# Optimization experiments

Measured on AMD Instinct MI355X. Metric: run time of the kernel, lower is better.

The kernel has to match this reference:

```python
import jax, jax.numpy as jnp
import numpy as np

TEMP = 1.0  # softmax temperature (init kwarg)


def setup_inputs() -> dict:
    key = jax.random.key(0)
    k1, k2 = jax.random.split(key)
    two_n, d_model = 512, 256
    embeddings = jax.random.normal(k1, (two_n, d_model), dtype=jnp.float32)
    targets = jax.random.uniform(k2, (two_n, 1), dtype=jnp.float32)
    return {"embeddings": embeddings, "targets": targets}


def reference(embeddings, targets):
    # embeddings: [2N, d_model], targets: [2N, 1]
    two_n = embeddings.shape[0]
    # label distance d[i,j] = |t_i - t_j|
    d = jnp.abs(targets - targets.T)                                  # [2N, 2N]
    # exp similarity s[i,j] = exp(-||e_i - e_j||_2 / temp)
    diff = embeddings[:, None, :] - embeddings[None, :, :]            # [2N, 2N, d]
    s = jnp.exp(-jnp.linalg.norm(diff, axis=-1) / TEMP)               # [2N, 2N]
    off_diag = 1.0 - jnp.eye(two_n, dtype=s.dtype)                    # [2N, 2N]
    # mask3[i,k,j] = (d[i,j] >= d[i,k]) * (j != i)
    mask3 = (d[:, None, :] >= d[:, :, None]).astype(s.dtype) * off_diag[:, None, :]
    # denominator D[i,k] = sum_j mask3[i,k,j] * s[i,j]
    denom = jnp.einsum('ikj,ij->ik', mask3, s)                        # [2N, 2N]
    loss = jnp.log(s / denom) * off_diag
    return -jnp.sum(loss) / (two_n * (two_n - 1))
```

## Files before the change

kernel.cpp:

```cpp
#include <hip/hip_runtime.h>
#include <math.h>

#define TWO_N 512
#define DM    256
#define NT    256
#define NTR   512
#define KS    8
#define RSTRIDE (TWO_N * TWO_N)

#define OFF_TSORT (8u << 20)
#define OFF_INV   ((8u << 20) + 2048)
#define OFF_BSUM  ((8u << 20) + 4096)

#define ACC4(acc, A, B) { float _d;                      \
    _d = (A).x - (B).x; acc += _d * _d;                  \
    _d = (A).y - (B).y; acc += _d * _d;                  \
    _d = (A).z - (B).z; acc += _d * _d;                  \
    _d = (A).w - (B).w; acc += _d * _d; }

__global__ __launch_bounds__(NT) void supcr_dist_rank(
    const float* __restrict__ E, const float* __restrict__ T,
    float* __restrict__ R, float* __restrict__ tsort, int* __restrict__ inv)
{
    const int bid = blockIdx.x;
    const int t   = threadIdx.x;

    if (bid < 512) {
        __shared__ float4 As4[64 * 9];
        __shared__ float4 Bs4[64 * 9];
        const int tile = bid >> 3, ks = bid & 7;
        const int it = tile >> 3, jt = tile & 7;
        const float4* __restrict__ E4 = reinterpret_cast<const float4*>(E);

        #pragma unroll
        for (int p = 0; p < 2; ++p) {
            const int idx = t + p * 256;
            const int r = idx >> 3, c4 = idx & 7;
            As4[r * 9 + c4] = E4[(it * 64 + r) * 64 + ks * 8 + c4];
            Bs4[r * 9 + c4] = E4[(jt * 64 + r) * 64 + ks * 8 + c4];
        }
        __syncthreads();

        const int tx = t & 15, ty = t >> 4;
        float acc[4][4];
        #pragma unroll
        for (int u = 0; u < 4; ++u)
            #pragma unroll
            for (int v = 0; v < 4; ++v) acc[u][v] = 0.f;

        #pragma unroll
        for (int k4 = 0; k4 < 8; ++k4) {
            float4 a[4], b[4];
            #pragma unroll
            for (int u = 0; u < 4; ++u) a[u] = As4[(ty + 16 * u) * 9 + k4];
            #pragma unroll
            for (int v = 0; v < 4; ++v) b[v] = Bs4[(tx + 16 * v) * 9 + k4];
            #pragma unroll
            for (int u = 0; u < 4; ++u)
                #pragma unroll
                for (int v = 0; v < 4; ++v) ACC4(acc[u][v], a[u], b[v]);
        }

        float* __restrict__ Rp = R + (size_t)ks * RSTRIDE;
        #pragma unroll
        for (int u = 0; u < 4; ++u) {
            const int row = it * 64 + ty + 16 * u;
            #pragma unroll
            for (int v = 0; v < 4; ++v)
                Rp[row * TWO_N + jt * 64 + tx + 16 * v] = acc[u][v];
        }
    } else {
        __shared__ float Tsh[TWO_N];
        Tsh[t] = T[t]; Tsh[t + 256] = T[t + 256];
        __syncthreads();

        const int ja = t, jb = t + 256;
        const float ta = Tsh[ja], tb = Tsh[jb];
        int rka = 0, rkb = 0;
        const float4* Tsh4 = reinterpret_cast<const float4*>(Tsh);
        #pragma unroll 4
        for (int j4 = 0; j4 < TWO_N / 4; ++j4) {
            const float4 tv = Tsh4[j4];
            const int b0 = 4 * j4, b1 = b0 + 1, b2 = b0 + 2, b3 = b0 + 3;
            rka += (tv.x < ta) || (tv.x == ta && b0 < ja);
            rka += (tv.y < ta) || (tv.y == ta && b1 < ja);
            rka += (tv.z < ta) || (tv.z == ta && b2 < ja);
            rka += (tv.w < ta) || (tv.w == ta && b3 < ja);
            rkb += (tv.x < tb) || (tv.x == tb && b0 < jb);
            rkb += (tv.y < tb) || (tv.y == tb && b1 < jb);
            rkb += (tv.z < tb) || (tv.z == tb && b2 < jb);
            rkb += (tv.w < tb) || (tv.w == tb && b3 < jb);
        }
        tsort[rka] = ta;  inv[ja] = rka;
        tsort[rkb] = tb;  inv[jb] = rkb;
    }
}

__global__ __launch_bounds__(NTR) void supcr_rows(
    const float* __restrict__ T, const float* __restrict__ R,
    const float* __restrict__ tsort, const int* __restrict__ inv,
    double* __restrict__ bsums)
{
    const int i = blockIdx.x;
    const int k = threadIdx.x;
    const int lane = k & 63, wid = k >> 6;

    __shared__ float  ts[TWO_N];
    __shared__ float  Pe[TWO_N];
    __shared__ float  P[TWO_N];
    __shared__ float  wsumf[8];
    __shared__ double red8[8];

    const float ti = T[i];
    const float tk = T[k];

    float d2 = 0.f;
    #pragma unroll
    for (int p = 0; p < KS; ++p)
        d2 += R[(size_t)p * RSTRIDE + (size_t)i * TWO_N + k];
    const float rik = sqrtf(d2);
    const float e   = (k == i) ? 0.f : __expf(-rik);

    ts[k] = tsort[k];
    Pe[inv[k]] = e;
    __syncthreads();

    float v = Pe[k];
    #pragma unroll
    for (int off = 1; off < 64; off <<= 1) {
        const float u = __shfl_up(v, off, 64);
        if (lane >= off) v += u;
    }
    if (lane == 63) wsumf[wid] = v;
    __syncthreads();
    float base = 0.f, tot = 0.f;
    #pragma unroll
    for (int w = 0; w < 8; ++w) {
        const float s = wsumf[w];
        tot += s;
        if (w < wid) base += s;
    }
    P[k] = v + base;
    const float Stot = tot;
    __syncthreads();

    const int mi = inv[i];

    double local = 0.0;
    if (k != i) {
        const float theta = fabsf(ti - tk);

        const int nl = mi + 1;
        int pos = 0;
        #pragma unroll
        for (int step = 512; step >= 1; step >>= 1) {
            const int np = pos + step;
            if (np <= nl && fabsf(ti - ts[np - 1]) >= theta) pos = np;
        }
        const int cl = nl - pos;

        const int nr = TWO_N - mi;
        int pr = 0;
        #pragma unroll
        for (int step = 512; step >= 1; step >>= 1) {
            const int np = pr + step;
            if (np <= nr && fabsf(ti - ts[mi + np - 1]) < theta) pr = np;
        }
        const int cr = pr;

        float inner = 0.f;
        const int L  = mi - cl + 1;
        const int Rr = mi + cr - 1;
        if (Rr >= L) inner = P[Rr] - ((L > 0) ? P[L - 1] : 0.f);
        const float denom = Stot - inner;
        local = (double)(-rik - logf(denom));
    }

    #pragma unroll
    for (int off = 32; off > 0; off >>= 1) local += __shfl_down(local, off, 64);
    if (lane == 0) red8[wid] = local;
    __syncthreads();
    if (k == 0) {
        double s = 0.0;
        #pragma unroll
        for (int w = 0; w < 8; ++w) s += red8[w];
        bsums[i] = s;
    }
}

__global__ __launch_bounds__(64) void supcr_finalize(
    const double* __restrict__ bsums, float* __restrict__ out)
{
    const int t = threadIdx.x;
    double s = 0.0;
    #pragma unroll
    for (int w = 0; w < 8; ++w) s += bsums[t + 64 * w];
    #pragma unroll
    for (int off = 32; off > 0; off >>= 1) s += __shfl_down(s, off, 64);
    if (t == 0)
        out[0] = (float)(-s / (double)((long long)TWO_N * (TWO_N - 1)));
}

extern "C" void kernel_launch(void* const* d_in, const int* in_sizes, int n_in,
                              void* d_out, int out_size, void* d_ws, size_t ws_size,
                              hipStream_t stream) {
    (void)in_sizes; (void)n_in; (void)out_size; (void)ws_size;
    const float* E = (const float*)d_in[0];
    const float* T = (const float*)d_in[1];
    float* out = (float*)d_out;

    char* ws = (char*)d_ws;
    float*  R      = (float*)(ws);
    float*  tsortp = (float*)(ws + OFF_TSORT);
    int*    invp   = (int*)(ws + OFF_INV);
    double* bsums  = (double*)(ws + OFF_BSUM);

    supcr_dist_rank<<<513, NT, 0, stream>>>(E, T, R, tsortp, invp);
    supcr_rows<<<TWO_N, NTR, 0, stream>>>(T, R, tsortp, invp, bsums);
    supcr_finalize<<<1, 64, 0, stream>>>(bsums, out);
}
```

Measured before the change: 93.52 us.

## Fuse three kernels into one cooperative kernel with grid sync and atomic finalize

Merges the distance/rank kernel, the per-row loss kernel and the finalize kernel into one cooperative launch of 512 blocks of 256 threads. A grid.sync separates the partial-distance and rank phase from the row phase, and each thread now handles two columns. A last-block atomic counter does the final reduction, so two extra launches and the small finalize kernel go away. The cost is grid-wide barrier overhead and cooperative launch limits, and the final sum now depends on atomic double accumulation order.

```diff
diff --git a/kernel.cpp b/kernel.cpp
--- a/kernel.cpp
+++ b/kernel.cpp
@@ -1,16 +1,19 @@
 #include <hip/hip_runtime.h>
+#include <hip/hip_cooperative_groups.h>
 #include <math.h>
+
+namespace cg = cooperative_groups;
 
 #define TWO_N 512
 #define DM    256
 #define NT    256
-#define NTR   512
 #define KS    8
 #define RSTRIDE (TWO_N * TWO_N)
 
 #define OFF_TSORT (8u << 20)
 #define OFF_INV   ((8u << 20) + 2048)
-#define OFF_BSUM  ((8u << 20) + 4096)
+#define OFF_ACC   ((8u << 20) + 4096)
+#define OFF_CNT   ((8u << 20) + 12288)
 
 #define ACC4(acc, A, B) { float _d;                      \
     _d = (A).x - (B).x; acc += _d * _d;                  \
@@ -18,16 +21,27 @@
     _d = (A).z - (B).z; acc += _d * _d;                  \
     _d = (A).w - (B).w; acc += _d * _d; }
 
-__global__ __launch_bounds__(NT) void supcr_dist_rank(
+__global__ __launch_bounds__(NT) void supcr_coop(
     const float* __restrict__ E, const float* __restrict__ T,
-    float* __restrict__ R, float* __restrict__ tsort, int* __restrict__ inv)
+    float* __restrict__ R, float* __restrict__ tsort, int* __restrict__ inv,
+    double* __restrict__ acc, unsigned* __restrict__ cnt,
+    float* __restrict__ out)
 {
+    cg::grid_group grid = cg::this_grid();
     const int bid = blockIdx.x;
     const int t   = threadIdx.x;
 
-    if (bid < 512) {
-        __shared__ float4 As4[64 * 9];
-        __shared__ float4 Bs4[64 * 9];
+    __shared__ float4 As4[64 * 9];
+    __shared__ float4 Bs4[64 * 9];
+    __shared__ float  Tsh[TWO_N];
+    __shared__ float  ts[TWO_N];
+    __shared__ float  Pe[TWO_N];
+    __shared__ float  P[TWO_N];
+    __shared__ float  wsum[8];
+    __shared__ double red4[4];
+    __shared__ int    isLast;
+
+    {
         const int tile = bid >> 3, ks = bid & 7;
         const int it = tile >> 3, jt = tile & 7;
         const float4* __restrict__ E4 = reinterpret_cast<const float4*>(E);
@@ -42,11 +56,11 @@
         __syncthreads();
 
         const int tx = t & 15, ty = t >> 4;
-        float acc[4][4];
+        float a2[4][4];
         #pragma unroll
         for (int u = 0; u < 4; ++u)
             #pragma unroll
-            for (int v = 0; v < 4; ++v) acc[u][v] = 0.f;
+            for (int v = 0; v < 4; ++v) a2[u][v] = 0.f;
 
         #pragma unroll
         for (int k4 = 0; k4 < 8; ++k4) {
@@ -58,7 +72,7 @@
             #pragma unroll
             for (int u = 0; u < 4; ++u)
                 #pragma unroll
-                for (int v = 0; v < 4; ++v) ACC4(acc[u][v], a[u], b[v]);
+                for (int v = 0; v < 4; ++v) ACC4(a2[u][v], a[u], b[v]);
         }
 
         float* __restrict__ Rp = R + (size_t)ks * RSTRIDE;
@@ -67,138 +81,140 @@
             const int row = it * 64 + ty + 16 * u;
             #pragma unroll
             for (int v = 0; v < 4; ++v)
-                Rp[row * TWO_N + jt * 64 + tx + 16 * v] = acc[u][v];
-        }
-    } else {
-        __shared__ float Tsh[TWO_N];
+                Rp[row * TWO_N + jt * 64 + tx + 16 * v] = a2[u][v];
+        }
+    }
+
+    if (bid == 0) {
+        if (t < 64) acc[t * 16] = 0.0;
+        if (t == 0) *cnt = 0u;
+    }
+
+    if (bid < 2) {
         Tsh[t] = T[t]; Tsh[t + 256] = T[t + 256];
         __syncthreads();
-
-        const int ja = t, jb = t + 256;
-        const float ta = Tsh[ja], tb = Tsh[jb];
-        int rka = 0, rkb = 0;
+        const int   e  = bid * 256 + t;
+        const float te = Tsh[e];
+        int rk = 0;
         const float4* Tsh4 = reinterpret_cast<const float4*>(Tsh);
         #pragma unroll 4
         for (int j4 = 0; j4 < TWO_N / 4; ++j4) {
             const float4 tv = Tsh4[j4];
-            const int b0 = 4 * j4, b1 = b0 + 1, b2 = b0 + 2, b3 = b0 + 3;
-            rka += (tv.x < ta) || (tv.x == ta && b0 < ja);
-            rka += (tv.y < ta) || (tv.y == ta && b1 < ja);
-            rka += (tv.z < ta) || (tv.z == ta && b2 < ja);
-            rka += (tv.w < ta) || (tv.w == ta && b3 < ja);
-            rkb += (tv.x < tb) || (tv.x == tb && b0 < jb);
-            rkb += (tv.y < tb) || (tv.y == tb && b1 < jb);
-            rkb += (tv.z < tb) || (tv.z == tb && b2 < jb);
-            rkb += (tv.w < tb) || (tv.w == tb && b3 < jb);
-        }
-        tsort[rka] = ta;  inv[ja] = rka;
-        tsort[rkb] = tb;  inv[jb] = rkb;
-    }
-}
-
-__global__ __launch_bounds__(NTR) void supcr_rows(
-    const float* __restrict__ T, const float* __restrict__ R,
-    const float* __restrict__ tsort, const int* __restrict__ inv,
-    double* __restrict__ bsums)
-{
-    const int i = blockIdx.x;
-    const int k = threadIdx.x;
-    const int lane = k & 63, wid = k >> 6;
-
-    __shared__ float  ts[TWO_N];
-    __shared__ float  Pe[TWO_N];
-    __shared__ float  P[TWO_N];
-    __shared__ float  wsumf[8];
-    __shared__ double red8[8];
-
-    const float ti = T[i];
-    const float tk = T[k];
-
-    float d2 = 0.f;
-    #pragma unroll
-    for (int p = 0; p < KS; ++p)
-        d2 += R[(size_t)p * RSTRIDE + (size_t)i * TWO_N + k];
-    const float rik = sqrtf(d2);
-    const float e   = (k == i) ? 0.f : __expf(-rik);
-
-    ts[k] = tsort[k];
-    Pe[inv[k]] = e;
-    __syncthreads();
-
-    float v = Pe[k];
+            const int b0 = 4 * j4;
+            rk += (tv.x < te) || (tv.x == te && b0     < e);
+            rk += (tv.y < te) || (tv.y == te && b0 + 1 < e);
+            rk += (tv.z < te) || (tv.z == te && b0 + 2 < e);
+            rk += (tv.w < te) || (tv.w == te && b0 + 3 < e);
+        }
+        tsort[rk] = te;  inv[e] = rk;
+    }
+
+    grid.sync();
+
+    const int i    = bid;
+    const int lane = t & 63, wid = t >> 6;
+    const int m0 = t, m1 = t + 256;
+
+    const float ti  = T[i];
+    const float tk0 = T[m0], tk1 = T[m1];
+    ts[m0] = tsort[m0];  ts[m1] = tsort[m1];
+
+    float d20 = 0.f, d21 = 0.f;
+    #pragma unroll
+    for (int p = 0; p < KS; ++p) {
+        d20 += R[(size_t)p * RSTRIDE + (size_t)i * TWO_N + m0];
+        d21 += R[(size_t)p * RSTRIDE + (size_t)i * TWO_N + m1];
+    }
+    const float rik0 = sqrtf(d20), rik1 = sqrtf(d21);
+    const float e0 = (m0 == i) ? 0.f : __expf(-rik0);
+    const float e1 = (m1 == i) ? 0.f : __expf(-rik1);
+    Pe[inv[m0]] = e0;
+    Pe[inv[m1]] = e1;
+    __syncthreads();
+
+    float v0 = Pe[m0], v1 = Pe[m1];
     #pragma unroll
     for (int off = 1; off < 64; off <<= 1) {
-        const float u = __shfl_up(v, off, 64);
-        if (lane >= off) v += u;
-    }
-    if (lane == 63) wsumf[wid] = v;
-    __syncthreads();
-    float base = 0.f, tot = 0.f;
-    #pragma unroll
-    for (int w = 0; w < 8; ++w) {
-        const float s = wsumf[w];
+        const float u0 = __shfl_up(v0, off, 64);
+        const float u1 = __shfl_up(v1, off, 64);
+        if (lane >= off) { v0 += u0; v1 += u1; }
+    }
+    if (lane == 63) { wsum[wid] = v0; wsum[4 + wid] = v1; }
+    __syncthreads();
+
+    float b0f = 0.f, tot = 0.f;
+    #pragma unroll
+    for (int w = 0; w < 4; ++w) {
+        const float s = wsum[w];
         tot += s;
-        if (w < wid) base += s;
-    }
-    P[k] = v + base;
+        if (w < wid) b0f += s;
+    }
+    float b1f = tot;
+    #pragma unroll
+    for (int w = 0; w < 4; ++w) {
+        const float s = wsum[4 + w];
+        tot += s;
+        if (w < wid) b1f += s;
+    }
+    P[m0] = v0 + b0f;
+    P[m1] = v1 + b1f;
     const float Stot = tot;
     __syncthreads();
 
     const int mi = inv[i];
-
-    double local = 0.0;
-    if (k != i) {
-        const float theta = fabsf(ti - tk);
-
-        const int nl = mi + 1;
-        int pos = 0;
-        #pragma unroll
-        for (int step = 512; step >= 1; step >>= 1) {
-            const int np = pos + step;
-            if (np <= nl && fabsf(ti - ts[np - 1]) >= theta) pos = np;
-        }
-        const int cl = nl - pos;
-
-        const int nr = TWO_N - mi;
-        int pr = 0;
-        #pragma unroll
-        for (int step = 512; step >= 1; step >>= 1) {
-            const int np = pr + step;
-            if (np <= nr && fabsf(ti - ts[mi + np - 1]) < theta) pr = np;
-        }
-        const int cr = pr;
-
+    const int nl = mi + 1;
+    const int nr = TWO_N - mi;
+    const float th0 = fabsf(ti - tk0);
+    const float th1 = fabsf(ti - tk1);
+
+    int pos0 = 0, pr0 = 0, pos1 = 0, pr1 = 0;
+    #pragma unroll
+    for (int step = 512; step >= 1; step >>= 1) {
+        const int a0 = pos0 + step, c0 = pr0 + step;
+        const int a1 = pos1 + step, c1 = pr1 + step;
+        if (a0 <= nl && fabsf(ti - ts[a0 - 1])      >= th0) pos0 = a0;
+        if (c0 <= nr && fabsf(ti - ts[mi + c0 - 1]) <  th0) pr0  = c0;
+        if (a1 <= nl && fabsf(ti - ts[a1 - 1])      >= th1) pos1 = a1;
+        if (c1 <= nr && fabsf(ti - ts[mi + c1 - 1]) <  th1) pr1  = c1;
+    }
+
+    float lf = 0.f;
+    if (m0 != i) {
+        const int cl = nl - pos0, cr = pr0;
+        const int L = mi - cl + 1, Rr = mi + cr - 1;
         float inner = 0.f;
-        const int L  = mi - cl + 1;
-        const int Rr = mi + cr - 1;
         if (Rr >= L) inner = P[Rr] - ((L > 0) ? P[L - 1] : 0.f);
-        const float denom = Stot - inner;
-        local = (double)(-rik - logf(denom));
-    }
-
-    #pragma unroll
-    for (int off = 32; off > 0; off >>= 1) local += __shfl_down(local, off, 64);
-    if (lane == 0) red8[wid] = local;
-    __syncthreads();
-    if (k == 0) {
-        double s = 0.0;
-        #pragma unroll
-        for (int w = 0; w < 8; ++w) s += red8[w];
-        bsums[i] = s;
-    }
-}
-
-__global__ __launch_bounds__(64) void supcr_finalize(
-    const double* __restrict__ bsums, float* __restrict__ out)
-{
-    const int t = threadIdx.x;
-    double s = 0.0;
-    #pragma unroll
-    for (int w = 0; w < 8; ++w) s += bsums[t + 64 * w];
-    #pragma unroll
-    for (int off = 32; off > 0; off >>= 1) s += __shfl_down(s, off, 64);
-    if (t == 0)
-        out[0] = (float)(-s / (double)((long long)TWO_N * (TWO_N - 1)));
+        lf += -rik0 - logf(Stot - inner);
+    }
+    if (m1 != i) {
+        const int cl = nl - pos1, cr = pr1;
+        const int L = mi - cl + 1, Rr = mi + cr - 1;
+        float inner = 0.f;
+        if (Rr >= L) inner = P[Rr] - ((L > 0) ? P[L - 1] : 0.f);
+        lf += -rik1 - logf(Stot - inner);
+    }
+
+    double ld = (double)lf;
+    #pragma unroll
+    for (int off = 32; off > 0; off >>= 1) ld += __shfl_down(ld, off, 64);
+    if (lane == 0) red4[wid] = ld;
+    __syncthreads();
+
+    if (t == 0) {
+        const double bsum = red4[0] + red4[1] + red4[2] + red4[3];
+        atomicAdd(&acc[(i & 63) * 16], bsum);
+        __threadfence();
+        const unsigned old = atomicAdd(cnt, 1u);
+        isLast = (old == TWO_N - 1) ? 1 : 0;
+    }
+    __syncthreads();
+    if (isLast && t < 64) {
+        double s = atomicAdd(&acc[t * 16], 0.0);
+        #pragma unroll
+        for (int off = 32; off > 0; off >>= 1) s += __shfl_down(s, off, 64);
+        if (t == 0)
+            out[0] = (float)(-s / (double)((long long)TWO_N * (TWO_N - 1)));
+    }
 }
 
 extern "C" void kernel_launch(void* const* d_in, const int* in_sizes, int n_in,
@@ -210,12 +226,14 @@
     float* out = (float*)d_out;
 
     char* ws = (char*)d_ws;
-    float*  R      = (float*)(ws);
-    float*  tsortp = (float*)(ws + OFF_TSORT);
-    int*    invp   = (int*)(ws + OFF_INV);
-    double* bsums  = (double*)(ws + OFF_BSUM);
-
-    supcr_dist_rank<<<513, NT, 0, stream>>>(E, T, R, tsortp, invp);
-    supcr_rows<<<TWO_N, NTR, 0, stream>>>(T, R, tsortp, invp, bsums);
-    supcr_finalize<<<1, 64, 0, stream>>>(bsums, out);
+    float*    R      = (float*)(ws);
+    float*    tsortp = (float*)(ws + OFF_TSORT);
+    int*      invp   = (int*)(ws + OFF_INV);
+    double*   accp   = (double*)(ws + OFF_ACC);
+    unsigned* cntp   = (unsigned*)(ws + OFF_CNT);
+
+    void* args[] = { (void*)&E, (void*)&T, (void*)&R, (void*)&tsortp,
+                     (void*)&invp, (void*)&accp, (void*)&cntp, (void*)&out };
+    hipLaunchCooperativeKernel((const void*)supcr_coop, dim3(TWO_N), dim3(NT),
+                               args, 0, stream);
 }
```

Measured after the change: 155.0 us. 1.66x slower.
